# Kernel tuning notes

Measured on AMD Instinct MI355X. Metric: run time of the kernel, lower is better.

## Reference

```python
import jax, jax.numpy as jnp
import numpy as np

N, D, C, K, M = 32768, 512, 64, 16, 128
DEPTH = 4            # log2(K): decision-tree depth per codebook
NODES = K - 1        # 15 internal tree nodes per codebook


def _build_selection_matrix():
    # Node i of the binary tree lives at level log2(i+1) and thresholds the
    # level-l selected dimension of its codebook.
    S = np.zeros((C * NODES, C * DEPTH), dtype=np.float32)
    base = np.zeros((NODES, DEPTH), dtype=np.float32)
    for i in range(NODES):
        base[i, int(np.log2(i + 1))] = 1.0
    for c in range(C):
        S[c * NODES:(c + 1) * NODES, c * DEPTH:(c + 1) * DEPTH] = base
    return S


def _build_bit_matrix():
    # Leaf k scores +1/-1 on each of its DEPTH ancestor nodes; the true leaf
    # attains the maximal score DEPTH.
    base = np.zeros((K, NODES), dtype=np.float32)
    for k in range(K):
        for l in range(DEPTH):
            node = (1 << l) - 1 + (k >> (DEPTH - l))   # ancestor at level l
            bit = (k >> (DEPTH - 1 - l)) & 1            # right(1)/left(0)
            base[k, node] = 1.0 if bit else -1.0
    B = np.zeros((C * K, C * NODES), dtype=np.float32)
    for c in range(C):
        B[c * K:(c + 1) * K, c * NODES:(c + 1) * NODES] = base
    return B


def setup_inputs() -> dict:
    key = jax.random.key(0)
    k1, k2, k3, k4 = jax.random.split(key, 4)
    I = jax.random.normal(k1, (N, D), jnp.float32)
    T = jax.random.normal(k2, (C * NODES,), jnp.float32) * 0.1   # thresholds
    L = jax.random.normal(k3, (M, C, K), jnp.float32)            # LUT
    dims = jnp.sort(jax.random.randint(k4, (C * DEPTH,), 0, D))  # selected cols
    S = jnp.asarray(_build_selection_matrix())
    B = jnp.asarray(_build_bit_matrix())
    temp = jnp.ones((1,), jnp.float32)
    return {"I": I, "T": T, "L": L, "S": S, "B": B, "dims": dims, "temp": temp}


def reference(I, T, L, S, B, dims, temp):
    t = temp[0]
    x_sel = I[:, dims]                                  # (N, C*DEPTH) gather
    h = x_sel @ S.T - T                                 # (N, C*NODES)
    tanh_h = jnp.tanh(h / t)
    # straight-through sign: forward sign(h), backward d(tanh(h/t))
    sign_ste = jnp.sign(h) - jax.lax.stop_gradient(tanh_h) + tanh_h
    b = sign_ste @ B.T                                  # (N, C*K) leaf scores
    soft = jax.nn.softmax(b.reshape(-1, C, K) / t, axis=2)
    hard = jax.nn.one_hot(jnp.argmax(soft, axis=2), K, dtype=soft.dtype)
    # straight-through one-hot encoding E: forward hard, backward soft
    E = hard - jax.lax.stop_gradient(soft) + soft       # (N, C, K)
    return jnp.einsum("nck,mck->nm", E, L)              # LUT gather-sum readout
```

## Files before the change

### kernel.cpp

```cpp
#include <hip/hip_runtime.h>

#define N_TOTAL 32768
#define D_DIM   512
#define C_DIM   64
#define M_DIM   128
#define NODES_  15
#define ROWS_B  128
#define NCHUNK  8

typedef unsigned short u16;
typedef unsigned int   u32;
typedef unsigned long long u64;
typedef unsigned char  u8;
typedef float  f32x4   __attribute__((ext_vector_type(4)));
typedef short  short8v __attribute__((ext_vector_type(8)));

#define WAIT_VM(N) asm volatile("s_waitcnt vmcnt(" #N ")" ::: "memory")

__device__ __forceinline__ u32 f2bf_bits(float f) {
    u32 u = __float_as_uint(f);
    return (u + 0x7FFFu + ((u >> 16) & 1u)) >> 16;
}

__device__ __forceinline__ void gload_lds16(const float* g, float* l) {
    __builtin_amdgcn_global_load_lds(
        (const __attribute__((address_space(1))) void*)g,
        (__attribute__((address_space(3))) void*)l, 16, 0, 0);
}

__global__ __launch_bounds__(256) void build_lbf(
    const float* __restrict__ L, u16* __restrict__ Lbf)
{
    int idx  = blockIdx.x * 256 + threadIdx.x;
    int lane = idx & 63;
    int ch   = (idx >> 6) & 31;
    int ct   = idx >> 11;
    int m  = ct * 16 + (lane & 15);
    int k0 = ch * 32 + ((lane >> 4) * 8);
    const float* src = L + (size_t)m * 1024 + k0;
    float4 a = *(const float4*)(src);
    float4 b = *(const float4*)(src + 4);
    u32 w0 = f2bf_bits(a.x) | (f2bf_bits(a.y) << 16);
    u32 w1 = f2bf_bits(a.z) | (f2bf_bits(a.w) << 16);
    u32 w2 = f2bf_bits(b.x) | (f2bf_bits(b.y) << 16);
    u32 w3 = f2bf_bits(b.z) | (f2bf_bits(b.w) << 16);
    *(uint4*)(Lbf + (size_t)idx * 8) = make_uint4(w0, w1, w2, w3);
}

__global__ __launch_bounds__(512, 2) void mega_kernel(
    const float* __restrict__ I,
    const float* __restrict__ T,
    const int* __restrict__ dims,
    const u16* __restrict__ Lbf,
    float* __restrict__ out)
{
    __shared__ float sI[2][16 * D_DIM];
    __shared__ float sT[C_DIM * NODES_];
    __shared__ u8    sC[C_DIM * 132];

    const int tid  = threadIdx.x;
    const int lane = tid & 63;
    const int wv   = tid >> 6;
    const int rowBase = blockIdx.x * ROWS_B;

    const int4 dml = ((const int4*)dims)[lane];

    auto issue = [&](int t) {
        const float* src = I + (size_t)(rowBase + t * 16 + wv * 2) * D_DIM;
        float* dst = &sI[t & 1][wv * 2 * D_DIM];
        #pragma unroll
        for (int i = 0; i < 4; ++i)
            gload_lds16(src + i * 256 + lane * 4, dst + i * 256);
    };

    const float* tc = sT + lane * NODES_;

    auto descend_write = [&](int t) {
        u32 pk = 0;
        #pragma unroll
        for (int rr = 0; rr < 2; ++rr) {
            const float* v = &sI[t & 1][(wv * 2 + rr) * D_DIM];
            float x0 = v[dml.x], x1 = v[dml.y], x2 = v[dml.z], x3 = v[dml.w];
            int node = 0, k = 0;
            int b0 = (x0 - tc[0] > 0.0f) ? 1 : 0;
            k = b0; node = 1 + b0;
            int b1 = (x1 - tc[node] > 0.0f) ? 1 : 0;
            k = (k << 1) | b1; node = (node << 1) + 1 + b1;
            int b2 = (x2 - tc[node] > 0.0f) ? 1 : 0;
            k = (k << 1) | b2; node = (node << 1) + 1 + b2;
            int b3 = (x3 - tc[node] > 0.0f) ? 1 : 0;
            k = (k << 1) | b3;
            pk |= (u32)k << (8 * rr);
        }
        *(u16*)(sC + lane * 132 + t * 16 + wv * 2) = (u16)pk;
    };

    issue(0); issue(1);
    for (int j = tid; j < C_DIM * NODES_; j += 512) sT[j] = T[j];
    __syncthreads();
    descend_write(0); issue(2);
    descend_write(1); issue(3);
    WAIT_VM(4); descend_write(2); issue(4);
    WAIT_VM(4); descend_write(3); issue(5);
    WAIT_VM(4); descend_write(4); issue(6);
    WAIT_VM(4); descend_write(5); issue(7);
    WAIT_VM(4); descend_write(6);
    WAIT_VM(0); descend_write(7);
    __syncthreads();

    const int l15     = lane & 15;
    const int clsLane = (lane >> 5) & 1;
    const int kb      = ((lane >> 4) & 1) * 8;

    f32x4 acc[8] = {};
    const u16* lbW = Lbf + ((size_t)wv * 32 * 64 + lane) * 8;

    #pragma unroll 4
    for (int ch = 0; ch < 32; ++ch) {
        union { uint4 u; short8v v; } b;
        b.u = *(const uint4*)(lbW + (size_t)ch * 64 * 8);
        const int cls = ch * 2 + clsLane;
        const u8* cb = sC + cls * 132;
        #pragma unroll
        for (int rt = 0; rt < 8; ++rt) {
            u32 cd = cb[rt * 16 + l15];
            u32 tt = cd - (u32)kb;
            u64 sv = 0x3F80ull << ((tt & 3) * 16);
            union { u64 d[2]; short8v v; } a;
            a.d[0] = (tt < 4) ? sv : 0ull;
            a.d[1] = (tt >= 4 && tt < 8) ? sv : 0ull;
            acc[rt] = __builtin_amdgcn_mfma_f32_16x16x32_bf16(
                          a.v, b.v, acc[rt], 0, 0, 0);
        }
    }

    #pragma unroll
    for (int rt = 0; rt < 8; ++rt) {
        int r0 = rowBase + rt * 16 + ((lane >> 4) << 2);
        float* o = out + (size_t)r0 * M_DIM + wv * 16 + l15;
        o[0 * M_DIM] = acc[rt][0];
        o[1 * M_DIM] = acc[rt][1];
        o[2 * M_DIM] = acc[rt][2];
        o[3 * M_DIM] = acc[rt][3];
    }
}

extern "C" void kernel_launch(void* const* d_in, const int* in_sizes, int n_in,
                              void* d_out, int out_size, void* d_ws, size_t ws_size,
                              hipStream_t stream) {
    const float* I    = (const float*)d_in[0];
    const float* T    = (const float*)d_in[1];
    const float* L    = (const float*)d_in[2];
    const int*   dims = (const int*)d_in[5];

    u16* Lbf = (u16*)d_ws;

    hipLaunchKernelGGL(build_lbf, dim3(64), dim3(256), 0, stream, L, Lbf);
    hipLaunchKernelGGL(mega_kernel, dim3(N_TOTAL / ROWS_B), dim3(512), 0, stream,
                       I, T, dims, Lbf, (float*)d_out);
}
```

Baseline: 126.7 us.

## Halve rows per block, keep thresholds and leaf codes in registers

Rows per block drop from 128 to 64, so the grid doubles, and the occupancy hint is raised to 4 blocks. The aim is better latency hiding and load balance across CUs. Per-codebook thresholds now sit in registers and the tree descent uses branchless selects instead of LDS-indexed lookups, which removes the threshold LDS staging and its barrier. Leaf codes are packed four per u32 in registers and written once, so the MFMA loop reads one word per chunk instead of per-row bytes. The trade-off is that each block re-reads the whole bf16 LUT over half as many rows, and the 64KB input staging buffer may cap real occupancy below the hint.

Result: slower. 132.0 us (+4.1%).

```diff
diff --git a/kernel.cpp b/kernel.cpp
--- a/kernel.cpp
+++ b/kernel.cpp
@@ -4,9 +4,7 @@
 #define D_DIM   512
 #define C_DIM   64
 #define M_DIM   128
-#define NODES_  15
-#define ROWS_B  128
-#define NCHUNK  8
+#define ROWS_B  64
 
 typedef unsigned short u16;
 typedef unsigned int   u32;
@@ -47,7 +45,7 @@
     *(uint4*)(Lbf + (size_t)idx * 8) = make_uint4(w0, w1, w2, w3);
 }
 
-__global__ __launch_bounds__(512, 2) void mega_kernel(
+__global__ __launch_bounds__(512, 4) void mega_kernel(
     const float* __restrict__ I,
     const float* __restrict__ T,
     const int* __restrict__ dims,
@@ -55,75 +53,78 @@
     float* __restrict__ out)
 {
     __shared__ float sI[2][16 * D_DIM];
-    __shared__ float sT[C_DIM * NODES_];
-    __shared__ u8    sC[C_DIM * 132];
+    __shared__ u8    sC[C_DIM * 68];
 
     const int tid  = threadIdx.x;
     const int lane = tid & 63;
     const int wv   = tid >> 6;
     const int rowBase = blockIdx.x * ROWS_B;
 
+    float tr[15];
+    #pragma unroll
+    for (int j = 0; j < 15; ++j) tr[j] = T[lane * 15 + j];
+
     const int4 dml = ((const int4*)dims)[lane];
 
     auto issue = [&](int t) {
         const float* src = I + (size_t)(rowBase + t * 16 + wv * 2) * D_DIM;
-        float* dst = &sI[t & 1][wv * 2 * D_DIM];
+        float* dst = &sI[t & 1][(wv * 2) * D_DIM];
         #pragma unroll
         for (int i = 0; i < 4; ++i)
             gload_lds16(src + i * 256 + lane * 4, dst + i * 256);
     };
 
-    const float* tc = sT + lane * NODES_;
+    u32 c4[2] = {0u, 0u};
 
-    auto descend_write = [&](int t) {
-        u32 pk = 0;
+    auto descend = [&](int t) {
         #pragma unroll
         for (int rr = 0; rr < 2; ++rr) {
             const float* v = &sI[t & 1][(wv * 2 + rr) * D_DIM];
             float x0 = v[dml.x], x1 = v[dml.y], x2 = v[dml.z], x3 = v[dml.w];
-            int node = 0, k = 0;
-            int b0 = (x0 - tc[0] > 0.0f) ? 1 : 0;
-            k = b0; node = 1 + b0;
-            int b1 = (x1 - tc[node] > 0.0f) ? 1 : 0;
-            k = (k << 1) | b1; node = (node << 1) + 1 + b1;
-            int b2 = (x2 - tc[node] > 0.0f) ? 1 : 0;
-            k = (k << 1) | b2; node = (node << 1) + 1 + b2;
-            int b3 = (x3 - tc[node] > 0.0f) ? 1 : 0;
-            k = (k << 1) | b3;
-            pk |= (u32)k << (8 * rr);
+            bool b0 = (x0 - tr[0]) > 0.0f;
+            float t1v = b0 ? tr[2] : tr[1];
+            bool b1 = (x1 - t1v) > 0.0f;
+            float t2v = b0 ? (b1 ? tr[6] : tr[5]) : (b1 ? tr[4] : tr[3]);
+            bool b2 = (x2 - t2v) > 0.0f;
+            float t3v = b0 ? (b1 ? (b2 ? tr[14] : tr[13]) : (b2 ? tr[12] : tr[11]))
+                           : (b1 ? (b2 ? tr[10] : tr[9])  : (b2 ? tr[8]  : tr[7]));
+            bool b3 = (x3 - t3v) > 0.0f;
+            int k = (((((int)b0 << 1) | (int)b1) << 1 | (int)b2) << 1) | (int)b3;
+            c4[rr] |= (u32)k << (8 * t);
         }
-        *(u16*)(sC + lane * 132 + t * 16 + wv * 2) = (u16)pk;
     };
 
     issue(0); issue(1);
-    for (int j = tid; j < C_DIM * NODES_; j += 512) sT[j] = T[j];
-    __syncthreads();
-    descend_write(0); issue(2);
-    descend_write(1); issue(3);
-    WAIT_VM(4); descend_write(2); issue(4);
-    WAIT_VM(4); descend_write(3); issue(5);
-    WAIT_VM(4); descend_write(4); issue(6);
-    WAIT_VM(4); descend_write(5); issue(7);
-    WAIT_VM(4); descend_write(6);
-    WAIT_VM(0); descend_write(7);
+    WAIT_VM(4);
+    descend(0); issue(2);
+    WAIT_VM(4);
+    descend(1); issue(3);
+    WAIT_VM(4);
+    descend(2);
+    WAIT_VM(0);
+    descend(3);
+
+    #pragma unroll
+    for (int rr = 0; rr < 2; ++rr)
+        *(u32*)(sC + lane * 68 + (wv * 2 + rr) * 4) = c4[rr];
     __syncthreads();
 
     const int l15     = lane & 15;
     const int clsLane = (lane >> 5) & 1;
     const int kb      = ((lane >> 4) & 1) * 8;
 
-    f32x4 acc[8] = {};
-    const u16* lbW = Lbf + ((size_t)wv * 32 * 64 + lane) * 8;
+    f32x4 acc[4] = {};
+    const u16* lbW = Lbf + ((size_t)(wv * 32) * 64 + lane) * 8;
 
     #pragma unroll 4
     for (int ch = 0; ch < 32; ++ch) {
         union { uint4 u; short8v v; } b;
         b.u = *(const uint4*)(lbW + (size_t)ch * 64 * 8);
         const int cls = ch * 2 + clsLane;
-        const u8* cb = sC + cls * 132;
+        const u32 codes4 = *(const u32*)(sC + cls * 68 + l15 * 4);
         #pragma unroll
-        for (int rt = 0; rt < 8; ++rt) {
-            u32 cd = cb[rt * 16 + l15];
+        for (int rt = 0; rt < 4; ++rt) {
+            u32 cd = (codes4 >> (8 * rt)) & 0xFFu;
             u32 tt = cd - (u32)kb;
             u64 sv = 0x3F80ull << ((tt & 3) * 16);
             union { u64 d[2]; short8v v; } a;
@@ -135,7 +136,7 @@
     }
 
     #pragma unroll
-    for (int rt = 0; rt < 8; ++rt) {
+    for (int rt = 0; rt < 4; ++rt) {
         int r0 = rowBase + rt * 16 + ((lane >> 4) << 2);
         float* o = out + (size_t)r0 * M_DIM + wv * 16 + l15;
         o[0 * M_DIM] = acc[rt][0];
```
